# Kernel tuning notes

Measured on AMD Instinct MI355X. Metric: run time of the kernel, lower is better.

The kernel has to match this reference:

```python
import jax, jax.numpy as jnp
import numpy as np

N_EMBD = 768
N_HEAD = 12
HEAD_DIM = N_EMBD // N_HEAD
N_FREE = 3
NEG = jnp.float32(-1e30)


def _piece_masks():
    """Static 64x64 boolean reachability masks for each chess piece type.
    mask[q, k] = True means query square q may attend to key square k.
    Self-attention (q == k) is always allowed so no row is fully masked."""
    sq = np.arange(64)
    r, c = sq // 8, sq % 8
    dr = r[None, :] - r[:, None]  # row(k) - row(q)
    dc = c[None, :] - c[:, None]
    adr, adc = np.abs(dr), np.abs(dc)
    eye = np.eye(64, dtype=bool)
    knight = ((adr == 1) & (adc == 2)) | ((adr == 2) & (adc == 1))
    bishop = (adr == adc) & (adr != 0)
    rook = ((adr == 0) ^ (adc == 0))
    queen = bishop | rook
    king = np.maximum(adr, adc) == 1
    pawn = (dr == 1) & (adc <= 1)  # one step forward + diagonal captures
    return {k: v | eye for k, v in dict(knight=knight, bishop=bishop, rook=rook,
                                        queen=queen, king=king, pawn=pawn).items()}

_PM = _piece_masks()
# head layout: 2 knight, 2 bishop, 2 rook, 1 queen, 1 king, 1 pawn, 3 free
_PIECE_ORDER = ['knight', 'knight', 'bishop', 'bishop', 'rook', 'rook',
                'queen', 'king', 'pawn']
_PIECE_BIAS = jnp.asarray(
    np.stack([np.where(_PM[p], 0.0, -1e30) for p in _PIECE_ORDER]).astype(np.float32))


def _rmsnorm(x):
    eps = jnp.asarray(jnp.finfo(x.dtype).eps, x.dtype)
    return x * jax.lax.rsqrt(jnp.mean(jnp.square(x), axis=-1, keepdims=True) + eps)


def setup_inputs() -> dict:
    key = jax.random.key(0)
    ks = jax.random.split(key, 6)
    B = 1024
    x = jax.random.normal(ks[0], (B, 64, N_EMBD), dtype=jnp.float32)
    scale = 0.02
    Wq = jax.random.normal(ks[1], (N_EMBD, N_EMBD), dtype=jnp.float32) * scale
    Wk = jax.random.normal(ks[2], (N_EMBD, N_EMBD), dtype=jnp.float32) * scale
    Wv = jax.random.normal(ks[3], (N_EMBD, N_EMBD), dtype=jnp.float32) * scale
    Wo = jax.random.normal(ks[4], (N_EMBD, N_EMBD), dtype=jnp.float32) * scale
    free_logits = jax.random.normal(ks[5], (N_FREE, 64, 64), dtype=jnp.float32) * scale
    return {"x": x, "Wq": Wq, "Wk": Wk, "Wv": Wv, "Wo": Wo,
            "free_logits": free_logits}


def reference(x, Wq, Wk, Wv, Wo, free_logits):
    B, T, C = x.shape  # T == 64
    def proj(W):
        return (x @ W).reshape(B, T, N_HEAD, HEAD_DIM).transpose(0, 2, 1, 3)
    q, k, v = proj(Wq), proj(Wk), proj(Wv)  # (B, H, 64, hd)
    q, k = _rmsnorm(q), _rmsnorm(k)
    # attention bias: fixed piece masks for heads 0..8, learnable log-sigmoid for free heads
    free_bias = jnp.log(jax.nn.sigmoid(free_logits) + 1e-6)  # (3, 64, 64)
    bias = jnp.concatenate([_PIECE_BIAS, free_bias], axis=0)  # (12, 64, 64)
    scale = 1.0 / jnp.sqrt(jnp.asarray(HEAD_DIM, x.dtype))
    scores = jnp.einsum('bhqd,bhkd->bhqk', q, k) * scale + bias[None]
    attn = jax.nn.softmax(scores, axis=-1)
    y = jnp.einsum('bhqk,bhkd->bhqd', attn, v)
    y = y.transpose(0, 2, 1, 3).reshape(B, T, C)
    return y @ Wo
```

## Files before the change

### kernel.cpp

```cpp
#include <hip/hip_runtime.h>
#include <hip/hip_bf16.h>

typedef __attribute__((ext_vector_type(8))) __bf16 bf16x8;
typedef __attribute__((ext_vector_type(4))) float f32x4;
typedef __attribute__((ext_vector_type(8))) unsigned short u16x8;
typedef __attribute__((ext_vector_type(4))) unsigned int u32x4;

#define DEVI static __device__ __forceinline__

DEVI unsigned short f2bf(float f) {
  unsigned u = __builtin_bit_cast(unsigned, f);
  u += 0x7fffu + ((u >> 16) & 1u);
  return (unsigned short)(u >> 16);
}

DEVI bf16x8 ldbf8(const void* p) {
  return __builtin_bit_cast(bf16x8, *(const u16x8*)p);
}

DEVI void gload_lds16(const void* g, void* l) {
  __builtin_amdgcn_global_load_lds(
      (const __attribute__((address_space(1))) void*)g,
      (__attribute__((address_space(3))) void*)l, 16, 0, 0);
}

__global__ __launch_bounds__(256)
void prep_x_kernel(const float* __restrict__ x, unsigned short* __restrict__ xb) {
  size_t i = (size_t)(blockIdx.x * 256 + threadIdx.x) * 8;
  const float4* s = (const float4*)(x + i);
  float4 a = s[0], b = s[1];
  u16x8 o;
  o[0] = f2bf(a.x); o[1] = f2bf(a.y); o[2] = f2bf(a.z); o[3] = f2bf(a.w);
  o[4] = f2bf(b.x); o[5] = f2bf(b.y); o[6] = f2bf(b.z); o[7] = f2bf(b.w);
  *(u16x8*)(xb + i) = o;
}

__global__ __launch_bounds__(256)
void prep_w_kernel(const float* __restrict__ Wq, const float* __restrict__ Wk,
                   const float* __restrict__ Wv, const float* __restrict__ Wo,
                   const float* __restrict__ fl,
                   unsigned short* __restrict__ wqkv,
                   unsigned short* __restrict__ wo_t,
                   float* __restrict__ fb) {
  const int NQKV = 2304 * 768;
  const int NO = 768 * 768;
  int idx = blockIdx.x * 256 + threadIdx.x;
  if (idx < NQKV) {
    int n = idx / 768, kk = idx - n * 768;
    int sel = n / 768;
    int col = n - sel * 768;
    const float* W = (sel == 0) ? Wq : (sel == 1) ? Wk : Wv;
    wqkv[idx] = f2bf(W[kk * 768 + col]);
  } else if (idx < NQKV + NO) {
    int j = idx - NQKV;
    int n = j / 768, kk = j - n * 768;
    wo_t[j] = f2bf(Wo[kk * 768 + n]);
  } else if (idx < NQKV + NO + 3 * 64 * 64) {
    int j = idx - NQKV - NO;
    float v = fl[j];
    fb[j] = logf(1.0f / (1.0f + expf(-v)) + 1e-6f);
  }
}

template <int MODE>
__global__ __launch_bounds__(256, 2)
void gemm_kernel(const unsigned short* __restrict__ A,
                 const unsigned short* __restrict__ Bt,
                 unsigned short* __restrict__ q_ws,
                 unsigned short* __restrict__ k_ws,
                 unsigned short* __restrict__ vt_ws,
                 float* __restrict__ out, int nbn, int cpx) {
  __shared__ __align__(16) unsigned short As[128 * 64];
  __shared__ __align__(16) unsigned short Bs[128 * 64];
  const int tid = threadIdx.x;
  const int lane = tid & 63, wv = tid >> 6;
  const int wr = wv >> 1, wc = wv & 1;
  const int fq = lane >> 4, fr = lane & 15;
  const int bid0 = blockIdx.x;
  const int bid = (bid0 & 7) * cpx + (bid0 >> 3);
  const int bn = bid % nbn, bm = bid / nbn;

  f32x4 acc[4][4];
#pragma unroll
  for (int i = 0; i < 4; ++i)
#pragma unroll
    for (int j = 0; j < 4; ++j)
#pragma unroll
      for (int e = 0; e < 4; ++e) acc[i][j][e] = 0.f;

  for (int kt = 0; kt < 12; ++kt) {
#pragma unroll
    for (int c = 0; c < 4; ++c) {
      int lin = c * 256 + tid;
      int row = lin >> 3;
      int cs = (lin & 7) ^ (row & 7);
      size_t srcA;
      if constexpr (MODE == 0) {
        srcA = ((size_t)(bm * 128 + row) * 1536) + kt * 128 + cs * 16;
      } else {
        int m = bm * 128 + row;
        srcA = ((size_t)((m >> 6) * 12 + kt) * 8192) + (size_t)(m & 63) * 128 + cs * 16;
      }
      gload_lds16((const char*)A + srcA, (char*)As + c * 4096 + wv * 1024);
      size_t srcB = ((size_t)(bn * 128 + row) * 1536) + kt * 128 + cs * 16;
      gload_lds16((const char*)Bt + srcB, (char*)Bs + c * 4096 + wv * 1024);
    }
    __syncthreads();
#pragma unroll
    for (int kk = 0; kk < 2; ++kk) {
      bf16x8 af[4], bfr[4];
#pragma unroll
      for (int i = 0; i < 4; ++i) {
        int row = wr * 64 + i * 16 + fr;
        af[i] = ldbf8((const char*)As + row * 128 + ((kk * 4 + fq) ^ (fr & 7)) * 16);
      }
#pragma unroll
      for (int j = 0; j < 4; ++j) {
        int row = wc * 64 + j * 16 + fr;
        bfr[j] = ldbf8((const char*)Bs + row * 128 + ((kk * 4 + fq) ^ (fr & 7)) * 16);
      }
#pragma unroll
      for (int i = 0; i < 4; ++i)
#pragma unroll
        for (int j = 0; j < 4; ++j)
          acc[i][j] = __builtin_amdgcn_mfma_f32_16x16x32_bf16(af[i], bfr[j], acc[i][j], 0, 0, 0);
    }
    __syncthreads();
  }

  if constexpr (MODE == 0) {
    const int ncb = bn * 128 + wc * 64;
    const int sector = ncb / 768;
    const int hh = (ncb % 768) >> 6;
#pragma unroll
    for (int i = 0; i < 4; ++i) {
      if (sector < 2) {
#pragma unroll
        for (int r = 0; r < 4; ++r) {
          float ss = 0.f;
#pragma unroll
          for (int j = 0; j < 4; ++j) { float v = acc[i][j][r]; ss += v * v; }
          ss += __shfl_xor(ss, 1);
          ss += __shfl_xor(ss, 2);
          ss += __shfl_xor(ss, 4);
          ss += __shfl_xor(ss, 8);
          float rms = rsqrtf(ss * 0.015625f + 1.1920929e-7f);
#pragma unroll
          for (int j = 0; j < 4; ++j) acc[i][j][r] *= rms;
        }
      }
#pragma unroll
      for (int r = 0; r < 4; ++r) {
        int m = bm * 128 + wr * 64 + i * 16 + fq * 4 + r;
        size_t base = (size_t)((m >> 6) * 12 + hh) * 4096;
        int t = m & 63;
#pragma unroll
        for (int j = 0; j < 4; ++j) {
          int d = j * 16 + fr;
          unsigned short v = f2bf(acc[i][j][r]);
          if (sector == 0) q_ws[base + t * 64 + d] = v;
          else if (sector == 1) k_ws[base + t * 64 + d] = v;
          else vt_ws[base + d * 64 + t] = v;
        }
      }
    }
  } else {
#pragma unroll
    for (int i = 0; i < 4; ++i)
#pragma unroll
      for (int r = 0; r < 4; ++r) {
        int m = bm * 128 + wr * 64 + i * 16 + fq * 4 + r;
        float* op = out + (size_t)m * 768 + bn * 128 + wc * 64 + fr;
#pragma unroll
        for (int j = 0; j < 4; ++j) op[j * 16] = acc[i][j][r];
      }
  }
}

DEVI float piece_bias(int h, int tq, int tk) {
  if (tq == tk) return 0.f;
  int rq = tq >> 3, cq = tq & 7;
  int rk = tk >> 3, ck = tk & 7;
  int dr = rk - rq, dc = ck - cq;
  int adr = dr < 0 ? -dr : dr, adc = dc < 0 ? -dc : dc;
  bool ok;
  if (h < 2)       ok = (adr == 1 && adc == 2) || (adr == 2 && adc == 1);
  else if (h < 4)  ok = (adr == adc);
  else if (h < 6)  ok = (adr == 0) != (adc == 0);
  else if (h == 6) ok = (adr == adc) || ((adr == 0) != (adc == 0));
  else if (h == 7) ok = (adr <= 1 && adc <= 1);
  else             ok = (dr == 1) && (adc <= 1);
  return ok ? 0.f : -1e30f;
}

__global__ __launch_bounds__(256, 4)
void attn_kernel(unsigned short* __restrict__ q_ws,
                 const unsigned short* __restrict__ k_ws,
                 const unsigned short* __restrict__ vt_ws,
                 const float* __restrict__ fb) {
  __shared__ __align__(16) unsigned short qs[4096];
  __shared__ __align__(16) unsigned short ks2[4096];
  __shared__ __align__(16) unsigned short vs[4096];
  __shared__ __align__(16) unsigned short ps[4096];
  const int bid = blockIdx.x;
  const int h = bid % 12;
  const int tid = threadIdx.x;
  const int lane = tid & 63, w = tid >> 6;
  const int fq = lane >> 4, fr = lane & 15;
  const size_t gb = (size_t)bid * 8192;

#pragma unroll
  for (int c = 0; c < 2; ++c) {
    int byte = (c * 256 + tid) * 16;
    int row = byte >> 7;
    int colb = byte & 127;
    int sw = (row << 7) | (colb ^ ((row & 7) << 4));
    u32x4 a = *(const u32x4*)((const char*)q_ws + gb + byte);
    u32x4 b = *(const u32x4*)((const char*)k_ws + gb + byte);
    u32x4 v = *(const u32x4*)((const char*)vt_ws + gb + byte);
    *(u32x4*)((char*)qs + sw) = a;
    *(u32x4*)((char*)ks2 + sw) = b;
    *(u32x4*)((char*)vs + sw) = v;
  }
  __syncthreads();

  f32x4 sacc[4];
#pragma unroll
  for (int j = 0; j < 4; ++j)
#pragma unroll
    for (int e = 0; e < 4; ++e) sacc[j][e] = 0.f;
#pragma unroll
  for (int kk = 0; kk < 2; ++kk) {
    int kbyte = kk * 64 + fq * 16;
    int rq = w * 16 + fr;
    bf16x8 af = ldbf8((const char*)qs + (rq << 7) + (kbyte ^ ((rq & 7) << 4)));
#pragma unroll
    for (int j = 0; j < 4; ++j) {
      int rk = j * 16 + fr;
      bf16x8 bf_ = ldbf8((const char*)ks2 + (rk << 7) + (kbyte ^ ((rk & 7) << 4)));
      sacc[j] = __builtin_amdgcn_mfma_f32_16x16x32_bf16(af, bf_, sacc[j], 0, 0, 0);
    }
  }

#pragma unroll
  for (int r = 0; r < 4; ++r) {
    int tq = w * 16 + fq * 4 + r;
    float s[4];
#pragma unroll
    for (int j = 0; j < 4; ++j) {
      int tk = j * 16 + fr;
      float bias = (h >= 9) ? fb[(h - 9) * 4096 + tq * 64 + tk] : piece_bias(h, tq, tk);
      s[j] = sacc[j][r] * 0.125f + bias;
    }
    float mx = fmaxf(fmaxf(s[0], s[1]), fmaxf(s[2], s[3]));
    mx = fmaxf(mx, __shfl_xor(mx, 1));
    mx = fmaxf(mx, __shfl_xor(mx, 2));
    mx = fmaxf(mx, __shfl_xor(mx, 4));
    mx = fmaxf(mx, __shfl_xor(mx, 8));
    float sum = 0.f;
#pragma unroll
    for (int j = 0; j < 4; ++j) { s[j] = __expf(s[j] - mx); sum += s[j]; }
    sum += __shfl_xor(sum, 1);
    sum += __shfl_xor(sum, 2);
    sum += __shfl_xor(sum, 4);
    sum += __shfl_xor(sum, 8);
    float inv = 1.f / sum;
#pragma unroll
    for (int j = 0; j < 4; ++j) {
      int tk = j * 16 + fr;
      *(unsigned short*)((char*)ps + (tq << 7) + ((tk * 2) ^ ((tq & 7) << 4))) =
          f2bf(s[j] * inv);
    }
  }
  __syncthreads();

  f32x4 yacc[4];
#pragma unroll
  for (int j = 0; j < 4; ++j)
#pragma unroll
    for (int e = 0; e < 4; ++e) yacc[j][e] = 0.f;
#pragma unroll
  for (int kk = 0; kk < 2; ++kk) {
    int kbyte = kk * 64 + fq * 16;
    int rp = w * 16 + fr;
    bf16x8 af = ldbf8((const char*)ps + (rp << 7) + (kbyte ^ ((rp & 7) << 4)));
#pragma unroll
    for (int j = 0; j < 4; ++j) {
      int rv = j * 16 + fr;
      bf16x8 bf_ = ldbf8((const char*)vs + (rv << 7) + (kbyte ^ ((rv & 7) << 4)));
      yacc[j] = __builtin_amdgcn_mfma_f32_16x16x32_bf16(af, bf_, yacc[j], 0, 0, 0);
    }
  }
#pragma unroll
  for (int r = 0; r < 4; ++r) {
    int tq = w * 16 + fq * 4 + r;
#pragma unroll
    for (int j = 0; j < 4; ++j) {
      int d = j * 16 + fr;
      q_ws[(size_t)bid * 4096 + tq * 64 + d] = f2bf(yacc[j][r]);
    }
  }
}

extern "C" void kernel_launch(void* const* d_in, const int* in_sizes, int n_in,
                              void* d_out, int out_size, void* d_ws, size_t ws_size,
                              hipStream_t stream) {
  const float* x  = (const float*)d_in[0];
  const float* Wq = (const float*)d_in[1];
  const float* Wk = (const float*)d_in[2];
  const float* Wv = (const float*)d_in[3];
  const float* Wo = (const float*)d_in[4];
  const float* fl = (const float*)d_in[5];
  float* out = (float*)d_out;

  char* ws = (char*)d_ws;
  unsigned short* wqkv = (unsigned short*)ws;
  unsigned short* wo_t = (unsigned short*)(ws + 3538944);
  float* fb = (float*)(ws + 3538944 + 1179648);
  char* big = ws + 3538944 + 1179648 + 49152;
  unsigned short* q_ws  = (unsigned short*)big;
  unsigned short* k_ws  = (unsigned short*)(big + 100663296ULL);
  unsigned short* vt_ws = (unsigned short*)(big + 201326592ULL);
  unsigned short* x_bf = (unsigned short*)d_out;

  prep_x_kernel<<<24576, 256, 0, stream>>>(x, x_bf);
  prep_w_kernel<<<9264, 256, 0, stream>>>(Wq, Wk, Wv, Wo, fl, wqkv, wo_t, fb);
  gemm_kernel<0><<<9216, 256, 0, stream>>>(x_bf, wqkv, q_ws, k_ws, vt_ws, nullptr, 18, 1152);
  attn_kernel<<<12288, 256, 0, stream>>>(q_ws, k_ws, vt_ws, fb);
  gemm_kernel<1><<<3072, 256, 0, stream>>>(q_ws, wo_t, nullptr, nullptr, nullptr, out, 6, 384);
}
```

Before: 866.6 us.

## Use 256x256 GEMM tiles with double-buffered LDS prefetch and priority boost

```diff
diff --git a/kernel.cpp b/kernel.cpp
--- a/kernel.cpp
+++ b/kernel.cpp
@@ -63,77 +63,89 @@
 }
 
 template <int MODE>
-__global__ __launch_bounds__(256, 2)
-void gemm_kernel(const unsigned short* __restrict__ A,
-                 const unsigned short* __restrict__ Bt,
-                 unsigned short* __restrict__ q_ws,
-                 unsigned short* __restrict__ k_ws,
-                 unsigned short* __restrict__ vt_ws,
-                 float* __restrict__ out, int nbn, int cpx) {
-  __shared__ __align__(16) unsigned short As[128 * 64];
-  __shared__ __align__(16) unsigned short Bs[128 * 64];
+__global__ __launch_bounds__(512, 2)
+void gemm256_kernel(const unsigned short* __restrict__ A,
+                    const unsigned short* __restrict__ Bt,
+                    unsigned short* __restrict__ q_ws,
+                    unsigned short* __restrict__ k_ws,
+                    unsigned short* __restrict__ vt_ws,
+                    float* __restrict__ out, int nbn, int cpx) {
+  __shared__ __align__(16) char lds[131072];
   const int tid = threadIdx.x;
   const int lane = tid & 63, wv = tid >> 6;
-  const int wr = wv >> 1, wc = wv & 1;
+  const int wm = wv >> 2, wn = wv & 3;
   const int fq = lane >> 4, fr = lane & 15;
   const int bid0 = blockIdx.x;
   const int bid = (bid0 & 7) * cpx + (bid0 >> 3);
   const int bn = bid % nbn, bm = bid / nbn;
 
-  f32x4 acc[4][4];
-#pragma unroll
-  for (int i = 0; i < 4; ++i)
+  f32x4 acc[8][4];
+#pragma unroll
+  for (int i = 0; i < 8; ++i)
 #pragma unroll
     for (int j = 0; j < 4; ++j)
 #pragma unroll
       for (int e = 0; e < 4; ++e) acc[i][j][e] = 0.f;
 
-  for (int kt = 0; kt < 12; ++kt) {
+  auto STAGE = [&](int kt, int buf) {
 #pragma unroll
     for (int c = 0; c < 4; ++c) {
-      int lin = c * 256 + tid;
+      int lin = c * 512 + tid;
       int row = lin >> 3;
       int cs = (lin & 7) ^ (row & 7);
       size_t srcA;
       if constexpr (MODE == 0) {
-        srcA = ((size_t)(bm * 128 + row) * 1536) + kt * 128 + cs * 16;
+        srcA = ((size_t)(bm * 256 + row) * 768 + kt * 64 + cs * 8) * 2;
       } else {
-        int m = bm * 128 + row;
-        srcA = ((size_t)((m >> 6) * 12 + kt) * 8192) + (size_t)(m & 63) * 128 + cs * 16;
-      }
-      gload_lds16((const char*)A + srcA, (char*)As + c * 4096 + wv * 1024);
-      size_t srcB = ((size_t)(bn * 128 + row) * 1536) + kt * 128 + cs * 16;
-      gload_lds16((const char*)Bt + srcB, (char*)Bs + c * 4096 + wv * 1024);
-    }
-    __syncthreads();
+        int m = bm * 256 + row;
+        srcA = (((size_t)(m >> 6) * 12 + kt) * 4096 + (size_t)(m & 63) * 64 + cs * 8) * 2;
+      }
+      gload_lds16((const char*)A + srcA, lds + buf * 65536 + c * 8192 + wv * 1024);
+      size_t srcB = ((size_t)(bn * 256 + row) * 768 + kt * 64 + cs * 8) * 2;
+      gload_lds16((const char*)Bt + srcB, lds + buf * 65536 + 32768 + c * 8192 + wv * 1024);
+    }
+  };
+
+  auto COMPUTE = [&](int buf) {
+    const char* Ab = lds + buf * 65536;
+    const char* Bb = lds + buf * 65536 + 32768;
 #pragma unroll
     for (int kk = 0; kk < 2; ++kk) {
-      bf16x8 af[4], bfr[4];
-#pragma unroll
-      for (int i = 0; i < 4; ++i) {
-        int row = wr * 64 + i * 16 + fr;
-        af[i] = ldbf8((const char*)As + row * 128 + ((kk * 4 + fq) ^ (fr & 7)) * 16);
-      }
-#pragma unroll
-      for (int j = 0; j < 4; ++j) {
-        int row = wc * 64 + j * 16 + fr;
-        bfr[j] = ldbf8((const char*)Bs + row * 128 + ((kk * 4 + fq) ^ (fr & 7)) * 16);
-      }
-#pragma unroll
-      for (int i = 0; i < 4; ++i)
+      int koff = ((kk * 4 + fq) ^ (fr & 7)) * 16;
+      bf16x8 b4[4];
+#pragma unroll
+      for (int j = 0; j < 4; ++j)
+        b4[j] = ldbf8(Bb + (wn * 64 + j * 16 + fr) * 128 + koff);
+#pragma unroll
+      for (int i = 0; i < 8; ++i) {
+        bf16x8 a_ = ldbf8(Ab + (wm * 128 + i * 16 + fr) * 128 + koff);
 #pragma unroll
         for (int j = 0; j < 4; ++j)
-          acc[i][j] = __builtin_amdgcn_mfma_f32_16x16x32_bf16(af[i], bfr[j], acc[i][j], 0, 0, 0);
-    }
-    __syncthreads();
-  }
+          acc[i][j] = __builtin_amdgcn_mfma_f32_16x16x32_bf16(a_, b4[j], acc[i][j], 0, 0, 0);
+      }
+    }
+  };
+
+  STAGE(0, 0);
+  for (int t = 0; t < 11; ++t) {
+    STAGE(t + 1, (t + 1) & 1);
+    asm volatile("s_waitcnt vmcnt(8)" ::: "memory");
+    asm volatile("s_barrier" ::: "memory");
+    __builtin_amdgcn_s_setprio(1);
+    COMPUTE(t & 1);
+    __builtin_amdgcn_s_setprio(0);
+    asm volatile("s_barrier" ::: "memory");
+  }
+  asm volatile("s_waitcnt vmcnt(0)" ::: "memory");
+  asm volatile("s_barrier" ::: "memory");
+  COMPUTE(1);
 
   if constexpr (MODE == 0) {
-    const int ncb = bn * 128 + wc * 64;
+    const int ncb = bn * 256 + wn * 64;
     const int sector = ncb / 768;
     const int hh = (ncb % 768) >> 6;
 #pragma unroll
-    for (int i = 0; i < 4; ++i) {
+    for (int i = 0; i < 8; ++i) {
       if (sector < 2) {
 #pragma unroll
         for (int r = 0; r < 4; ++r) {
@@ -151,7 +163,7 @@
       }
 #pragma unroll
       for (int r = 0; r < 4; ++r) {
-        int m = bm * 128 + wr * 64 + i * 16 + fq * 4 + r;
+        int m = bm * 256 + wm * 128 + i * 16 + fq * 4 + r;
         size_t base = (size_t)((m >> 6) * 12 + hh) * 4096;
         int t = m & 63;
 #pragma unroll
@@ -166,11 +178,11 @@
     }
   } else {
 #pragma unroll
-    for (int i = 0; i < 4; ++i)
+    for (int i = 0; i < 8; ++i)
 #pragma unroll
       for (int r = 0; r < 4; ++r) {
-        int m = bm * 128 + wr * 64 + i * 16 + fq * 4 + r;
-        float* op = out + (size_t)m * 768 + bn * 128 + wc * 64 + fr;
+        int m = bm * 256 + wm * 128 + i * 16 + fq * 4 + r;
+        float* op = out + (size_t)m * 768 + bn * 256 + wn * 64 + fr;
 #pragma unroll
         for (int j = 0; j < 4; ++j) op[j * 16] = acc[i][j][r];
       }
@@ -325,7 +337,7 @@
 
   prep_x_kernel<<<24576, 256, 0, stream>>>(x, x_bf);
   prep_w_kernel<<<9264, 256, 0, stream>>>(Wq, Wk, Wv, Wo, fl, wqkv, wo_t, fb);
-  gemm_kernel<0><<<9216, 256, 0, stream>>>(x_bf, wqkv, q_ws, k_ws, vt_ws, nullptr, 18, 1152);
+  gemm256_kernel<0><<<2304, 512, 0, stream>>>(x_bf, wqkv, q_ws, k_ws, vt_ws, nullptr, 9, 288);
   attn_kernel<<<12288, 256, 0, stream>>>(q_ws, k_ws, vt_ws, fb);
-  gemm_kernel<1><<<3072, 256, 0, stream>>>(q_ws, wo_t, nullptr, nullptr, nullptr, out, 6, 384);
-}
+  gemm256_kernel<1><<<768, 512, 0, stream>>>(q_ws, wo_t, nullptr, nullptr, nullptr, out, 3, 96);
+}
```

Result: slower. 899.7 us (+3.8%).
